# Performance work log

Hardware: AMD Instinct MI355X
Metric: run time of the kernel (lower is better)

## Reference

```python
import jax, jax.numpy as jnp
import numpy as np
import math

WS = 7          # window side
NH = 4          # num heads
CIN = 128       # in_channels
HD = CIN // NH  # head dim
SCALE = 1.0 / math.sqrt(HD)


def _rel_index():
    # standard Swin relative-position index, [WS*WS, WS*WS]
    c = np.stack(np.meshgrid(np.arange(WS), np.arange(WS), indexing='ij'), 0).reshape(2, -1)
    r = (c[:, :, None] - c[:, None, :]).transpose(1, 2, 0)  # [n, n, 2]
    r[..., 0] += WS - 1
    r[..., 1] += WS - 1
    r[..., 0] *= 2 * WS - 1
    return r.sum(-1)


def setup_inputs() -> dict:
    key = jax.random.key(0)
    ks = jax.random.split(key, 12)
    B, C, H, W = 64, CIN, 56, 56
    s = 0.02
    return {
        'query': jax.random.normal(ks[0], (B, C, H, W), jnp.float32),
        'key': jax.random.normal(ks[1], (B, C, H, W), jnp.float32),
        'value': jax.random.normal(ks[2], (B, C, H, W), jnp.float32),
        'Wq': jax.random.normal(ks[3], (C, C), jnp.float32) * s,
        'bq': jnp.zeros((C,), jnp.float32),
        'Wk': jax.random.normal(ks[4], (C, C), jnp.float32) * s,
        'bk': jnp.zeros((C,), jnp.float32),
        'Wv': jax.random.normal(ks[5], (C, C), jnp.float32) * s,
        'bv': jnp.zeros((C,), jnp.float32),
        'Wo': jax.random.normal(ks[6], (C, C), jnp.float32) * s,
        'bo': jnp.zeros((C,), jnp.float32),
        'rpb_table': jax.random.normal(ks[7], ((2 * WS - 1) ** 2, NH), jnp.float32) * s,
    }


def reference(query, key, value, Wq, bq, Wk, bk, Wv, bv, Wo, bo, rpb_table):
    B, C, H, W = query.shape
    nh, nw = H // WS, W // WS
    n = WS * WS

    def to_seq(x):
        # [B, C, H, W] -> [(B*nh*nw), n, C] window partition
        x = x.reshape(B, C, nh, WS, nw, WS)
        return x.transpose(0, 2, 4, 3, 5, 1).reshape(B * nh * nw, n, C)

    def to_spatial(x):
        x = x.reshape(B, nh, nw, WS, WS, C)
        return x.transpose(0, 5, 1, 3, 2, 4).reshape(B, C, H, W)

    q = to_seq(query) @ Wq.T + bq
    k = to_seq(key) @ Wk.T + bk
    v = to_seq(value) @ Wv.T + bv

    def heads(x):
        return x.reshape(-1, n, NH, HD).transpose(0, 2, 1, 3)  # [b, h, n, d]

    q, k, v = heads(q), heads(k), heads(v)

    score = jnp.einsum('bhid,bhjd->bhij', q, k) * SCALE
    idx = _rel_index()  # static numpy [n, n]
    bias = rpb_table[idx.reshape(-1)].reshape(n, n, NH).transpose(2, 0, 1)  # [h, n, n]
    score = score + bias[None]
    ctx = jax.nn.softmax(score, axis=-1)
    out = jnp.einsum('bhij,bhjd->bhid', ctx, v)
    out = out.transpose(0, 2, 1, 3).reshape(-1, n, C)
    x = out @ Wo.T + bo
    return to_spatial(x), ctx
```

## Files before the change

### kernel.cpp

```cpp
#include <hip/hip_runtime.h>

#define NTOK 49
#define CC   128
#define NHEADS 4
#define HWW  56
#define HW2  3136
#define SCALE_F 0.17677669529663687f

typedef __attribute__((ext_vector_type(8))) short s16x8;
typedef __attribute__((ext_vector_type(4))) float f32x4;
typedef __attribute__((ext_vector_type(16))) float f32x16;
typedef __attribute__((ext_vector_type(2))) unsigned int u32x2;

static __device__ __forceinline__ unsigned short f2bf(float f) {
  unsigned int u = __float_as_uint(f);
  u += 0x7fffu + ((u >> 16) & 1u);
  return (unsigned short)(u >> 16);
}
static __device__ __forceinline__ float bf2f(unsigned short h) {
  return __uint_as_float(((unsigned int)h) << 16);
}
static __device__ __forceinline__ unsigned int cvtpk(float lo, float hi) {
  unsigned int r;
  asm("v_cvt_pk_bf16_f32 %0, %1, %2" : "=v"(r) : "v"(lo), "v"(hi));
  return r;
}
static __device__ __forceinline__ int swz8(int row, int col) { return col ^ ((row & 7) << 3); }

union FragU { s16x8 v; unsigned int u[4]; };

__global__ void prep_kernel(const float* __restrict__ Wq, const float* __restrict__ Wk,
                            const float* __restrict__ Wv, const float* __restrict__ Wo,
                            const float* __restrict__ rpb,
                            unsigned short* __restrict__ dstW, float* __restrict__ dstB) {
  int i = blockIdx.x * 256 + threadIdx.x;
  if (i < 65536) {
    const float* src = (i < 16384) ? Wq : (i < 32768) ? Wk : (i < 49152) ? Wv : Wo;
    float v = src[i & 16383];
    if (i < 16384) v *= SCALE_F;
    dstW[i] = f2bf(v);
  } else {
    int j = i - 65536;
    if (j < NHEADS*NTOK*NTOK) {
      int h = j / (NTOK*NTOK), rem = j - h*(NTOK*NTOK);
      int k = rem / NTOK, q = rem - k*NTOK;
      int qi = q/7, qj = q - qi*7, ki = k/7, kj = k - ki*7;
      dstB[j] = rpb[((qi-ki+6)*13 + (qj-kj+6))*NHEADS + h];
    }
  }
}

__global__ __launch_bounds__(256, 3)
void winattn_kernel(const float* __restrict__ Xq, const float* __restrict__ Xk,
                    const float* __restrict__ Xv,
                    const unsigned short* __restrict__ Wbf,
                    const float* __restrict__ Biasg,
                    const float* __restrict__ bq, const float* __restrict__ bk,
                    const float* __restrict__ bv, const float* __restrict__ bo,
                    float* __restrict__ out_x,
                    float* __restrict__ out_ctx)
{
  __shared__ alignas(16) unsigned short smem[26368];
  unsigned short* Buf0 = smem;
  unsigned short* Buf1 = smem + 6272;
  unsigned short* VT   = smem + 12544;
  unsigned short* Buf2 = smem + 19712;
  float* Obnc = (float*)(smem + 12544);

  const int tid = threadIdx.x;
  const int wv  = tid >> 6;
  const int l   = tid & 63;
  const int lr  = l & 15;
  const int lg  = l >> 4;
  const int c31 = l & 31;
  const int hi  = l >> 5;

  const int win  = (blockIdx.x & 7) * 512 + (blockIdx.x >> 3);
  const int bimg = win >> 6;
  const int r0   = ((win >> 3) & 7) * 7;
  const int c0   = (win & 7) * 7;

  {
    unsigned int* vz = (unsigned int*)VT;
    #pragma unroll
    for (int i = 0; i < 14; ++i) vz[tid + i*256] = 0u;
    int s = tid & 63, g = tid >> 6;
    if (s < NTOK) {
      int si = s / 7, sj = s - si*7;
      size_t base = (size_t)bimg*CC*HW2 + (size_t)(r0+si)*HWW + (c0+sj);
      #pragma unroll 4
      for (int cp = 0; cp < 8; ++cp) {
        int ci = g*32 + cp*4;
        size_t off = base + (size_t)ci * HW2;
        float q0 = Xq[off], q1 = Xq[off+HW2], q2 = Xq[off+2*HW2], q3 = Xq[off+3*HW2];
        float k0 = Xk[off], k1 = Xk[off+HW2], k2 = Xk[off+2*HW2], k3 = Xk[off+3*HW2];
        float v0 = Xv[off], v1 = Xv[off+HW2], v2 = Xv[off+2*HW2], v3 = Xv[off+3*HW2];
        int di = s*CC + swz8(s, ci);
        u32x2 pq = {cvtpk(q0,q1), cvtpk(q2,q3)};
        u32x2 pk = {cvtpk(k0,k1), cvtpk(k2,k3)};
        u32x2 pv = {cvtpk(v0,v1), cvtpk(v2,v3)};
        *(u32x2*)(Buf0 + di) = pq;
        *(u32x2*)(Buf1 + di) = pk;
        *(u32x2*)(Buf2 + di) = pv;
      }
    }
  }
  __syncthreads();

  auto projR = [&](const unsigned short* __restrict__ src, const unsigned short* __restrict__ Wg,
                   const float* __restrict__ bias, float bscale,
                   f32x4 (&acc)[4][2], float (&bb)[2]) {
    s16x8 bfr[2][4];
    #pragma unroll
    for (int ntl = 0; ntl < 2; ++ntl) {
      int col = wv*32 + ntl*16 + lr;
      bb[ntl] = bias[col] * bscale;
      #pragma unroll
      for (int ks = 0; ks < 4; ++ks)
        bfr[ntl][ks] = *(const s16x8*)(Wg + col*CC + ks*32 + lg*8);
    }
    #pragma unroll
    for (int mt = 0; mt < 4; ++mt) {
      int ar = mt*16 + lr;
      s16x8 af[4];
      #pragma unroll
      for (int ks = 0; ks < 4; ++ks)
        af[ks] = *(const s16x8*)(src + ar*CC + swz8(ar, ks*32 + lg*8));
      #pragma unroll
      for (int ntl = 0; ntl < 2; ++ntl) {
        f32x4 a = {0.f,0.f,0.f,0.f};
        #pragma unroll
        for (int ks = 0; ks < 4; ++ks)
          a = __builtin_amdgcn_mfma_f32_16x16x32_bf16(af[ks], bfr[ntl][ks], a, 0,0,0);
        acc[mt][ntl] = a;
      }
    }
  };
  auto projW = [&](unsigned short* __restrict__ dst, f32x4 (&acc)[4][2], float (&bb)[2]) {
    #pragma unroll
    for (int mt = 0; mt < 4; ++mt) {
      #pragma unroll
      for (int ntl = 0; ntl < 2; ++ntl) {
        int col = wv*32 + ntl*16 + lr;
        int row0 = mt*16 + lg*4;
        unsigned int p01 = cvtpk(acc[mt][ntl][0]+bb[ntl], acc[mt][ntl][1]+bb[ntl]);
        unsigned int p23 = cvtpk(acc[mt][ntl][2]+bb[ntl], acc[mt][ntl][3]+bb[ntl]);
        if (row0   < NTOK) dst[ row0   *CC + swz8(row0,  col)] = (unsigned short)p01;
        if (row0+1 < NTOK) dst[(row0+1)*CC + swz8(row0+1,col)] = (unsigned short)(p01>>16);
        if (row0+2 < NTOK) dst[(row0+2)*CC + swz8(row0+2,col)] = (unsigned short)p23;
        if (row0+3 < NTOK) dst[(row0+3)*CC + swz8(row0+3,col)] = (unsigned short)(p23>>16);
      }
    }
  };

  f32x4 acc[4][2]; float bb[2];
  projR(Buf0, Wbf, bq, SCALE_F, acc, bb);
  __syncthreads();
  projW(Buf0, acc, bb);
  projR(Buf1, Wbf + 16384, bk, 1.f, acc, bb);
  __syncthreads();
  projW(Buf1, acc, bb);
  {
    s16x8 bfr[2][4]; float vb[2];
    #pragma unroll
    for (int ntl = 0; ntl < 2; ++ntl) {
      int col = wv*32 + ntl*16 + lr;
      vb[ntl] = bv[col];
      #pragma unroll
      for (int ks = 0; ks < 4; ++ks)
        bfr[ntl][ks] = *(const s16x8*)(Wbf + 32768 + col*CC + ks*32 + lg*8);
    }
    #pragma unroll
    for (int mt = 0; mt < 4; ++mt) {
      int ar = mt*16 + lr;
      s16x8 af[4];
      #pragma unroll
      for (int ks = 0; ks < 4; ++ks)
        af[ks] = *(const s16x8*)(Buf2 + ar*CC + swz8(ar, ks*32 + lg*8));
      #pragma unroll
      for (int ntl = 0; ntl < 2; ++ntl) {
        f32x4 a = {0.f,0.f,0.f,0.f};
        #pragma unroll
        for (int ks = 0; ks < 4; ++ks)
          a = __builtin_amdgcn_mfma_f32_16x16x32_bf16(af[ks], bfr[ntl][ks], a, 0,0,0);
        int col = wv*32 + ntl*16 + lr;
        int row0 = mt*16 + lg*4;
        unsigned int p01 = cvtpk(a[0]+vb[ntl], a[1]+vb[ntl]);
        unsigned int p23 = cvtpk(a[2]+vb[ntl], a[3]+vb[ntl]);
        int vbse = col*56 + row0;
        if (row0+1 < NTOK) *(unsigned int*)(VT + vbse) = p01;
        else if (row0 < NTOK) VT[vbse] = (unsigned short)p01;
        if (row0+3 < NTOK) *(unsigned int*)(VT + vbse + 2) = p23;
        else if (row0+2 < NTOK) VT[vbse+2] = (unsigned short)p23;
      }
    }
  }
  __syncthreads();

  {
    const int h = wv;
    const float* Bh = Biasg + h*(NTOK*NTOK);
    s16x8 ak[2][2], av[4];
    #pragma unroll
    for (int kt = 0; kt < 2; ++kt) {
      int krow = kt*32 + c31; if (krow > 48) krow = 48;
      #pragma unroll
      for (int ks = 0; ks < 2; ++ks)
        ak[kt][ks] = *(const s16x8*)(Buf1 + krow*CC + swz8(krow, h*32 + ks*16 + hi*8));
    }
    #pragma unroll
    for (int kk = 0; kk < 4; ++kk)
      av[kk] = *(const s16x8*)(VT + (h*32 + c31)*56 + kk*16 + hi*8);
    size_t cbase = ((size_t)win*NHEADS + h)*(NTOK*NTOK);
    unsigned short* PL = Buf2 + h*1664;

    #pragma unroll
    for (int qh = 0; qh < 2; ++qh) {
      int q = qh*32 + c31;
      int qrow = q > 48 ? 48 : q;
      s16x8 bqf[2];
      #pragma unroll
      for (int ks = 0; ks < 2; ++ks)
        bqf[ks] = *(const s16x8*)(Buf0 + qrow*CC + swz8(qrow, h*32 + ks*16 + hi*8));
      f32x16 s0 = {0,0,0,0,0,0,0,0,0,0,0,0,0,0,0,0};
      f32x16 s1 = {0,0,0,0,0,0,0,0,0,0,0,0,0,0,0,0};
      __builtin_amdgcn_s_setprio(1);
      s0 = __builtin_amdgcn_mfma_f32_32x32x16_bf16(ak[0][0], bqf[0], s0, 0,0,0);
      s0 = __builtin_amdgcn_mfma_f32_32x32x16_bf16(ak[0][1], bqf[1], s0, 0,0,0);
      s1 = __builtin_amdgcn_mfma_f32_32x32x16_bf16(ak[1][0], bqf[0], s1, 0,0,0);
      s1 = __builtin_amdgcn_mfma_f32_32x32x16_bf16(ak[1][1], bqf[1], s1, 0,0,0);
      __builtin_amdgcn_s_setprio(0);
      float mx = -1e30f;
      #pragma unroll
      for (int r = 0; r < 16; ++r) {
        int kb = (r&3) + 8*(r>>2) + 4*hi;
        float v0 = -1e30f, v1 = -1e30f;
        if (q < NTOK) {
          v0 = s0[r] + Bh[kb*NTOK + q];
          if (kb + 32 < NTOK) v1 = s1[r] + Bh[(kb+32)*NTOK + q];
        }
        s0[r] = v0; mx = fmaxf(mx, v0);
        s1[r] = v1; mx = fmaxf(mx, v1);
      }
      mx = fmaxf(mx, __shfl_xor(mx, 32));
      float sum = 0.f;
      #pragma unroll
      for (int r = 0; r < 16; ++r) { s0[r] = __expf(s0[r]-mx); sum += s0[r]; }
      #pragma unroll
      for (int r = 0; r < 16; ++r) { s1[r] = __expf(s1[r]-mx); sum += s1[r]; }
      sum += __shfl_xor(sum, 32);
      float rinv = 1.f / sum;
      #pragma unroll
      for (int r = 0; r < 16; ++r) { s0[r] *= rinv; s1[r] *= rinv; }
      if (q < NTOK) {
        #pragma unroll
        for (int g = 0; g < 4; ++g) {
          u32x2 w;
          w[0] = cvtpk(s0[4*g],   s0[4*g+1]);
          w[1] = cvtpk(s0[4*g+2], s0[4*g+3]);
          *(u32x2*)(PL + c31*52 + g*8 + 4*hi) = w;
          int k2 = g*8 + 4*hi + 32;
          if (k2 <= 48) {
            u32x2 w2;
            w2[0] = cvtpk(s1[4*g],   s1[4*g+1]);
            w2[1] = cvtpk(s1[4*g+2], s1[4*g+3]);
            *(u32x2*)(PL + c31*52 + k2) = w2;
          }
        }
      }
      f32x16 pacc = {0,0,0,0,0,0,0,0,0,0,0,0,0,0,0,0};
      auto pvstep = [&](f32x16& e, const s16x8& a0, const s16x8& a1) {
        unsigned int w0m0 = cvtpk(e[0],e[1]),   w0m1 = cvtpk(e[2],e[3]);
        unsigned int w1m0 = cvtpk(e[4],e[5]),   w1m1 = cvtpk(e[6],e[7]);
        unsigned int w2m0 = cvtpk(e[8],e[9]),   w2m1 = cvtpk(e[10],e[11]);
        unsigned int w3m0 = cvtpk(e[12],e[13]), w3m1 = cvtpk(e[14],e[15]);
        unsigned int p0m0 = __shfl_xor((int)w0m0,32), p0m1 = __shfl_xor((int)w0m1,32);
        unsigned int p1m0 = __shfl_xor((int)w1m0,32), p1m1 = __shfl_xor((int)w1m1,32);
        unsigned int p2m0 = __shfl_xor((int)w2m0,32), p2m1 = __shfl_xor((int)w2m1,32);
        unsigned int p3m0 = __shfl_xor((int)w3m0,32), p3m1 = __shfl_xor((int)w3m1,32);
        FragU f;
        f.u[0] = hi ? p1m0 : w0m0;  f.u[1] = hi ? p1m1 : w0m1;
        f.u[2] = hi ? w1m0 : p0m0;  f.u[3] = hi ? w1m1 : p0m1;
        __builtin_amdgcn_s_setprio(1);
        pacc = __builtin_amdgcn_mfma_f32_32x32x16_bf16(a0, f.v, pacc, 0,0,0);
        __builtin_amdgcn_s_setprio(0);
        f.u[0] = hi ? p3m0 : w2m0;  f.u[1] = hi ? p3m1 : w2m1;
        f.u[2] = hi ? w3m0 : p2m0;  f.u[3] = hi ? w3m1 : p2m1;
        __builtin_amdgcn_s_setprio(1);
        pacc = __builtin_amdgcn_mfma_f32_32x32x16_bf16(a1, f.v, pacc, 0,0,0);
        __builtin_amdgcn_s_setprio(0);
      };
      pvstep(s0, av[0], av[1]);
      pvstep(s1, av[2], av[3]);
      {
        const int cnt = (qh == 0) ? 32*NTOK : 17*NTOK;
        size_t gb = cbase + (size_t)qh*32*NTOK;
        #pragma unroll
        for (int base = 0; base < 32*NTOK; base += 64) {
          int idx = base + l;
          if (idx < cnt) {
            int qq = idx / NTOK, kk2 = idx - qq*NTOK;
            out_ctx[gb + idx] = bf2f(PL[qq*52 + kk2]);
          }
        }
      }
      if (q < NTOK) {
        #pragma unroll
        for (int r = 0; r < 16; ++r) {
          int d = (r&3) + 8*(r>>2) + 4*hi;
          Buf0[q*CC + swz8(q, h*32 + d)] = f2bf(pacc[r]);
        }
      }
    }
  }
  __syncthreads();

  {
    const unsigned short* Wg = Wbf + 49152;
    float* Of = Obnc + wv*1600;
    s16x8 bfr[2][4]; float ob[2];
    #pragma unroll
    for (int ntl = 0; ntl < 2; ++ntl) {
      int col = wv*32 + ntl*16 + lr;
      ob[ntl] = bo[col];
      #pragma unroll
      for (int ks = 0; ks < 4; ++ks)
        bfr[ntl][ks] = *(const s16x8*)(Wg + col*CC + ks*32 + lg*8);
    }
    #pragma unroll
    for (int mt = 0; mt < 4; ++mt) {
      int ar = mt*16 + lr;
      s16x8 af[4];
      #pragma unroll
      for (int ks = 0; ks < 4; ++ks)
        af[ks] = *(const s16x8*)(Buf0 + ar*CC + swz8(ar, ks*32 + lg*8));
      #pragma unroll
      for (int ntl = 0; ntl < 2; ++ntl) {
        f32x4 a = {0.f,0.f,0.f,0.f};
        #pragma unroll
        for (int ks = 0; ks < 4; ++ks)
          a = __builtin_amdgcn_mfma_f32_16x16x32_bf16(af[ks], bfr[ntl][ks], a, 0,0,0);
        #pragma unroll
        for (int r = 0; r < 4; ++r) {
          int row = mt*16 + lg*4 + r;
          if (row < NTOK)
            Of[(ntl*16 + lr)*50 + row] = a[r] + ob[ntl];
        }
      }
    }
    int chb = bimg*CC + wv*32;
    #pragma unroll
    for (int it = 0; it < 25; ++it) {
      int e = it*64 + l;
      if (e < 32*NTOK) {
        int ch = e / NTOK, tok = e - ch*NTOK;
        int si = tok / 7, sj = tok - si*7;
        out_x[(size_t)(chb + ch)*HW2 + (size_t)(r0+si)*HWW + (c0+sj)] = Of[ch*50 + tok];
      }
    }
  }
}

extern "C" void kernel_launch(void* const* d_in, const int* in_sizes, int n_in,
                              void* d_out, int out_size, void* d_ws, size_t ws_size,
                              hipStream_t stream) {
  (void)in_sizes; (void)n_in; (void)out_size; (void)ws_size;
  const float* query = (const float*)d_in[0];
  const float* key   = (const float*)d_in[1];
  const float* value = (const float*)d_in[2];
  const float* Wq = (const float*)d_in[3];
  const float* bq = (const float*)d_in[4];
  const float* Wk = (const float*)d_in[5];
  const float* bk = (const float*)d_in[6];
  const float* Wv = (const float*)d_in[7];
  const float* bv = (const float*)d_in[8];
  const float* Wo = (const float*)d_in[9];
  const float* bo = (const float*)d_in[10];
  const float* rpb = (const float*)d_in[11];

  unsigned short* Wbf = (unsigned short*)d_ws;
  float* Biasg = (float*)((char*)d_ws + 131072);
  float* out_x   = (float*)d_out;
  float* out_ctx = out_x + (size_t)64*CC*HW2;

  prep_kernel<<<294, 256, 0, stream>>>(Wq, Wk, Wv, Wo, rpb, Wbf, Biasg);
  winattn_kernel<<<4096, 256, 0, stream>>>(query, key, value, Wbf, Biasg,
                                           bq, bk, bv, bo, out_x, out_ctx);
}
```

Baseline: 269.1 us.

## Reorder projections to cut barriers, widen LDS swizzle, merge setprio regions

The V projection now runs first through the shared projR helper. The Q and K projections are then both computed into registers before a single barrier and written back together, which removes one __syncthreads. The LDS swizzle also XORs in bit 3 of the row to reduce bank conflicts across 16-row groups. The two PV MFMAs share one raised-priority region instead of two. The cost is higher register pressure from holding the Q and K accumulators live at the same time, which could lower occupancy.

```diff
diff --git a/kernel.cpp b/kernel.cpp
--- a/kernel.cpp
+++ b/kernel.cpp
@@ -25,7 +25,9 @@
   asm("v_cvt_pk_bf16_f32 %0, %1, %2" : "=v"(r) : "v"(lo), "v"(hi));
   return r;
 }
-static __device__ __forceinline__ int swz8(int row, int col) { return col ^ ((row & 7) << 3); }
+static __device__ __forceinline__ int swz8(int row, int col) {
+  return col ^ ((row & 7) << 3) ^ ((row & 8) << 3);
+}
 
 union FragU { s16x8 v; unsigned int u[4]; };
 
@@ -153,40 +155,17 @@
     }
   };
 
-  f32x4 acc[4][2]; float bb[2];
-  projR(Buf0, Wbf, bq, SCALE_F, acc, bb);
-  __syncthreads();
-  projW(Buf0, acc, bb);
-  projR(Buf1, Wbf + 16384, bk, 1.f, acc, bb);
-  __syncthreads();
-  projW(Buf1, acc, bb);
   {
-    s16x8 bfr[2][4]; float vb[2];
-    #pragma unroll
-    for (int ntl = 0; ntl < 2; ++ntl) {
-      int col = wv*32 + ntl*16 + lr;
-      vb[ntl] = bv[col];
-      #pragma unroll
-      for (int ks = 0; ks < 4; ++ks)
-        bfr[ntl][ks] = *(const s16x8*)(Wbf + 32768 + col*CC + ks*32 + lg*8);
-    }
+    f32x4 accV[4][2]; float bbV[2];
+    projR(Buf2, Wbf + 32768, bv, 1.f, accV, bbV);
     #pragma unroll
     for (int mt = 0; mt < 4; ++mt) {
-      int ar = mt*16 + lr;
-      s16x8 af[4];
-      #pragma unroll
-      for (int ks = 0; ks < 4; ++ks)
-        af[ks] = *(const s16x8*)(Buf2 + ar*CC + swz8(ar, ks*32 + lg*8));
       #pragma unroll
       for (int ntl = 0; ntl < 2; ++ntl) {
-        f32x4 a = {0.f,0.f,0.f,0.f};
-        #pragma unroll
-        for (int ks = 0; ks < 4; ++ks)
-          a = __builtin_amdgcn_mfma_f32_16x16x32_bf16(af[ks], bfr[ntl][ks], a, 0,0,0);
         int col = wv*32 + ntl*16 + lr;
         int row0 = mt*16 + lg*4;
-        unsigned int p01 = cvtpk(a[0]+vb[ntl], a[1]+vb[ntl]);
-        unsigned int p23 = cvtpk(a[2]+vb[ntl], a[3]+vb[ntl]);
+        unsigned int p01 = cvtpk(accV[mt][ntl][0]+bbV[ntl], accV[mt][ntl][1]+bbV[ntl]);
+        unsigned int p23 = cvtpk(accV[mt][ntl][2]+bbV[ntl], accV[mt][ntl][3]+bbV[ntl]);
         int vbse = col*56 + row0;
         if (row0+1 < NTOK) *(unsigned int*)(VT + vbse) = p01;
         else if (row0 < NTOK) VT[vbse] = (unsigned short)p01;
@@ -195,6 +174,12 @@
       }
     }
   }
+  f32x4 accQ[4][2], accK[4][2]; float bbQ[2], bbK[2];
+  projR(Buf0, Wbf,         bq, SCALE_F, accQ, bbQ);
+  projR(Buf1, Wbf + 16384, bk, 1.f,     accK, bbK);
+  __syncthreads();
+  projW(Buf0, accQ, bbQ);
+  projW(Buf1, accK, bbK);
   __syncthreads();
 
   {
@@ -283,10 +268,8 @@
         f.u[2] = hi ? w1m0 : p0m0;  f.u[3] = hi ? w1m1 : p0m1;
         __builtin_amdgcn_s_setprio(1);
         pacc = __builtin_amdgcn_mfma_f32_32x32x16_bf16(a0, f.v, pacc, 0,0,0);
-        __builtin_amdgcn_s_setprio(0);
         f.u[0] = hi ? p3m0 : w2m0;  f.u[1] = hi ? p3m1 : w2m1;
         f.u[2] = hi ? w3m0 : p2m0;  f.u[3] = hi ? w3m1 : p2m1;
-        __builtin_amdgcn_s_setprio(1);
         pacc = __builtin_amdgcn_mfma_f32_32x32x16_bf16(a1, f.v, pacc, 0,0,0);
         __builtin_amdgcn_s_setprio(0);
       };
```

After: 274.9 us. 2.1% more time.
